# Kernel optimization log

Measured on AMD Instinct MI355X. Metric: run time of the kernel, lower is better.

The kernel has to match this reference:

```python
import jax, jax.numpy as jnp
import numpy as np

N = 4096; E = 32768; S = 64; V = 16; H0 = 64; H1 = 16; STEPS = 3
SQRT3 = float(np.sqrt(3.0))


def _tp(sx, vx, sy, vy):
    # full CG tensor product restricted to paths landing in 0e/1o
    # sx [n,m0], vx [n,m1,3], sy [n,k0], vy [n,k1,3]
    n = sx.shape[0]
    ss = (sx[:, :, None] * sy[:, None, :]).reshape(n, -1)              # 0e x 0e -> 0e
    dd = (jnp.einsum('nmi,nki->nmk', vx, vy) / SQRT3).reshape(n, -1)    # 1o . 1o -> 0e
    sv = (sx[:, :, None, None] * vy[:, None, :, :]).reshape(n, -1, 3)   # 0e x 1o -> 1o
    vs = (vx[:, :, None, :] * sy[:, None, :, None]).reshape(n, -1, 3)   # 1o x 0e -> 1o
    return jnp.concatenate([ss, dd], -1), jnp.concatenate([sv, vs], -2)


def _tpl_gate(sx, vx, sy, vy, ws, b, wv, n0):
    # TensorProductLinearGate: tensor_product -> Linear -> gate
    s_tp, v_tp = _tp(sx, vx, sy, vy)
    s = s_tp @ ws + b                                  # scalars + gate scalars
    v = jnp.einsum('ntd,tm->nmd', v_tp, wv)
    scal = jax.nn.gelu(s[:, :n0])
    gates = jax.nn.sigmoid(s[:, n0:])
    return scal, v * gates[:, :, None]


def _seg_mean(x, idx, n):
    s = jax.ops.segment_sum(x, idx, num_segments=n)
    c = jax.ops.segment_sum(jnp.ones((x.shape[0],), x.dtype), idx, num_segments=n)
    c = jnp.maximum(c, 1.0).reshape((n,) + (1,) * (x.ndim - 1))
    return s / c


def setup_inputs() -> dict:
    key = jax.random.key(0)
    ks = jax.random.split(key, 20)
    f32 = jnp.float32

    def w(k, shape):
        return jax.random.normal(k, shape, f32) / np.sqrt(shape[-2]).astype(np.float32)

    def bias(k, shape):
        return 0.1 * jax.random.normal(k, shape, f32)

    E1 = 2 * (S + V)          # 160: edge block0 TP width
    E2 = H0 + H1              # 80: edge blocks 1-2 TP width
    K0 = H0 + 1; K1 = H1 + 1  # message concat sh
    N0TP = S * K0 + V * K1    # 4432
    N1TP = S * K1 + V * K0    # 2128
    return {
        'node_s': jax.random.normal(ks[0], (N, S), f32),
        'node_v': jax.random.normal(ks[1], (N, V, 3), f32),
        'senders': jax.random.randint(ks[2], (E,), 0, N, jnp.int32),
        'receivers': jax.random.randint(ks[3], (E,), 0, N, jnp.int32),
        'e1_ws': w(ks[4], (STEPS, E1, H0 + H1)),
        'e1_b': bias(ks[5], (STEPS, H0 + H1)),
        'e1_wv': w(ks[6], (STEPS, E1, H1)),
        'e2_ws': w(ks[7], (STEPS, 2, E2, H0 + H1)),
        'e2_b': bias(ks[8], (STEPS, 2, H0 + H1)),
        'e2_wv': w(ks[9], (STEPS, 2, E2, H1)),
        'n_ws': w(ks[10], (STEPS, 3, N0TP, S + V)),
        'n_b': bias(ks[11], (STEPS, 3, S + V)),
        'n_wv': w(ks[12], (STEPS, 3, N1TP, V)),
        'l_ws': w(ks[13], (STEPS, S, S)),
        'l_b': bias(ks[14], (STEPS, S)),
        'l_wv': w(ks[15], (STEPS, V, V)),
    }


def reference(node_s, node_v, senders, receivers, e1_ws, e1_b, e1_wv,
              e2_ws, e2_b, e2_wv, n_ws, n_b, n_wv, l_ws, l_b, l_wv):
    norm = float(E - 1)
    for step in range(STEPS):
        s_i, v_i = node_s[senders], node_v[senders]
        s_j, v_j = node_s[receivers], node_v[receivers]
        r = v_i[:, 0] - v_j[:, 0]                    # slice_by_mul[:1] = positions
        rn = jnp.linalg.norm(r, axis=-1, keepdims=True)
        unit = r / jnp.maximum(rn, 1e-9)
        a_s = jnp.ones((E, 1), node_s.dtype)          # Y_0, component norm
        a_v = (SQRT3 * unit)[:, None, :]              # Y_1, component norm
        m_s = jnp.concatenate([s_i, s_j], -1)
        m_v = jnp.concatenate([v_i, v_j], -2)
        for blk in range(3):
            if blk == 0:
                ws, b, wv = e1_ws[step], e1_b[step], e1_wv[step]
            else:
                ws, b, wv = e2_ws[step, blk - 1], e2_b[step, blk - 1], e2_wv[step, blk - 1]
            m_s, m_v = _tpl_gate(m_s, m_v, a_s, a_v, ws, b, wv, H0)
        # ---- aggregate (segment_mean) + normalize_messages ----
        ms = _seg_mean(m_s, receivers, N) / norm
        mv = _seg_mean(m_v, receivers, N) / norm
        as_ = _seg_mean(a_s, receivers, N) / norm
        av = _seg_mean(a_v, receivers, N) / norm
        y_s = jnp.concatenate([ms, as_], -1)          # [N, H0+1]
        y_v = jnp.concatenate([mv, av], -2)           # [N, H1+1, 3]
        for blk in range(3):
            node_s, node_v = _tpl_gate(node_s, node_v, y_s, y_v,
                                       n_ws[step, blk], n_b[step, blk], n_wv[step, blk], S)
        # ---- final per-step Linear(irreps_in) ----
        node_s = node_s @ l_ws[step] + l_b[step]
        node_v = jnp.einsum('nmd,mk->nkd', node_v, l_wv[step])
    return jnp.concatenate([node_v.reshape(node_v.shape[0], -1), node_s], -1)
```

## Files before the change

kernel.cpp:

```cpp
#include <hip/hip_runtime.h>
#include <math.h>

constexpr int NND = 4096;
constexpr int EDG = 32768;
constexpr float SQRT3  = 1.7320508075688772f;
constexpr float ISQRT3 = 0.5773502691896258f;
constexpr float NORMI  = 1.0f / 32767.0f;

__device__ __forceinline__ float gelu_f(float x) {
    float x3 = x * x * x;
    return 0.5f * x * (1.0f + tanhf(0.7978845608028654f * (x + 0.044715f * x3)));
}
__device__ __forceinline__ float sigmoid_f(float x) {
    return 1.0f / (1.0f + expf(-x));
}

__global__ __launch_bounds__(256)
void segnn_deg_kernel(const int* __restrict__ rcv, int* __restrict__ deg) {
    const int e = blockIdx.x * 256 + threadIdx.x;
    if (e < EDG) atomicAdd(deg + rcv[e], 1);
}

__global__ __launch_bounds__(1024)
void segnn_scan_kernel(const int* __restrict__ deg, int* __restrict__ off) {
    __shared__ int tots[1024];
    const int t = threadIdx.x;
    const int v0 = deg[4*t], v1 = deg[4*t+1], v2 = deg[4*t+2], v3 = deg[4*t+3];
    const int p1 = v0, p2 = p1 + v1, p3 = p2 + v2, p4 = p3 + v3;
    tots[t] = p4;
    __syncthreads();
    for (int d = 1; d < 1024; d <<= 1) {
        const int add = (t >= d) ? tots[t - d] : 0;
        __syncthreads();
        tots[t] += add;
        __syncthreads();
    }
    const int excl = t ? tots[t-1] : 0;
    off[4*t+0] = excl;
    off[4*t+1] = excl + p1;
    off[4*t+2] = excl + p2;
    off[4*t+3] = excl + p3;
    if (t == 1023) off[4096] = tots[1023];
}

__global__ __launch_bounds__(256)
void segnn_scatter_kernel(const int* __restrict__ rcv, const int* __restrict__ off,
                          int* __restrict__ cursor, int* __restrict__ elist) {
    const int e = blockIdx.x * 256 + threadIdx.x;
    if (e < EDG) {
        const int j = rcv[e];
        const int p = atomicAdd(cursor + j, 1);
        elist[off[j] + p] = e;
    }
}

template<int NSX, int NVX>
__device__ __forceinline__ void edge_phase_w(
    const int lane,
    const float* __restrict__ Ws, const float* __restrict__ Bs,
    const float* __restrict__ Wv,
    float (*xt)[10], float (*x2)[10], float (*cb)[96], float (*cvv)[48])
{
    const int cs = lane & 15, kg = lane >> 4;
    constexpr int KA = NSX + NVX;
    constexpr int CH = KA / 4;

    {
        float acc[8][6];
#pragma unroll
        for (int j = 0; j < 8; ++j)
#pragma unroll
            for (int c = 0; c < 6; ++c) acc[j][c] = 0.0f;
        const int r0 = kg * CH;
#pragma unroll 4
        for (int rr = 0; rr < CH; ++rr) {
            const int r = r0 + rr;
            const float* wp = Ws + r*80 + cs;
            const float w0 = wp[0], w1 = wp[16], w2 = wp[32], w3 = wp[48], w4 = wp[64];
            const float w5 = (r < NSX) ? Wv[r*16 + cs] : 0.0f;
            const float2 xa = *reinterpret_cast<const float2*>(&xt[r][0]);
            const float2 xb = *reinterpret_cast<const float2*>(&xt[r][2]);
            const float2 xc = *reinterpret_cast<const float2*>(&xt[r][4]);
            const float2 xd = *reinterpret_cast<const float2*>(&xt[r][6]);
            const float xe[8] = { xa.x,xa.y, xb.x,xb.y, xc.x,xc.y, xd.x,xd.y };
#pragma unroll
            for (int j = 0; j < 8; ++j) {
                acc[j][0] = fmaf(xe[j], w0, acc[j][0]);
                acc[j][1] = fmaf(xe[j], w1, acc[j][1]);
                acc[j][2] = fmaf(xe[j], w2, acc[j][2]);
                acc[j][3] = fmaf(xe[j], w3, acc[j][3]);
                acc[j][4] = fmaf(xe[j], w4, acc[j][4]);
                acc[j][5] = fmaf(xe[j], w5, acc[j][5]);
            }
        }
#pragma unroll
        for (int j = 0; j < 8; ++j)
#pragma unroll
            for (int c = 0; c < 6; ++c) {
                float a = acc[j][c];
                a += __shfl_xor(a, 16);
                a += __shfl_xor(a, 32);
                acc[j][c] = a;
            }
        if (lane < 16) {
#pragma unroll
            for (int j = 0; j < 8; ++j) {
#pragma unroll
                for (int c = 0; c < 5; ++c) cb[j][cs + 16*c] = acc[j][c] + Bs[cs + 16*c];
                cb[j][80 + cs] = acc[j][5];
            }
        }
    }

    {
        constexpr int CHB = NVX / 4;
        float av[8][3];
#pragma unroll
        for (int j = 0; j < 8; ++j) { av[j][0]=0.0f; av[j][1]=0.0f; av[j][2]=0.0f; }
        const int m0 = kg * CHB;
#pragma unroll
        for (int mm = 0; mm < CHB; ++mm) {
            const int m = m0 + mm;
            const float w = Wv[(NSX + m)*16 + cs];
#pragma unroll
            for (int d = 0; d < 3; ++d) {
                const float2 xa = *reinterpret_cast<const float2*>(&x2[d*NVX + m][0]);
                const float2 xb = *reinterpret_cast<const float2*>(&x2[d*NVX + m][2]);
                const float2 xc = *reinterpret_cast<const float2*>(&x2[d*NVX + m][4]);
                const float2 xd = *reinterpret_cast<const float2*>(&x2[d*NVX + m][6]);
                const float xe[8] = { xa.x,xa.y, xb.x,xb.y, xc.x,xc.y, xd.x,xd.y };
#pragma unroll
                for (int j = 0; j < 8; ++j) av[j][d] = fmaf(xe[j], w, av[j][d]);
            }
        }
#pragma unroll
        for (int j = 0; j < 8; ++j)
#pragma unroll
            for (int d = 0; d < 3; ++d) {
                float a = av[j][d];
                a += __shfl_xor(a, 16);
                a += __shfl_xor(a, 32);
                av[j][d] = a;
            }
        if (lane < 16) {
#pragma unroll
            for (int j = 0; j < 8; ++j)
#pragma unroll
                for (int d = 0; d < 3; ++d) cvv[j][cs*3 + d] = av[j][d];
        }
    }
    asm volatile("" ::: "memory");
}

__global__ __launch_bounds__(256, 2)
void segnn_edge_fused(const float* __restrict__ cs, const float* __restrict__ cv,
                      const int* __restrict__ snd, const int* __restrict__ rcv,
                      const float* __restrict__ W0s, const float* __restrict__ B0, const float* __restrict__ W0v,
                      const float* __restrict__ W1s, const float* __restrict__ B1, const float* __restrict__ W1v,
                      const float* __restrict__ W2s, const float* __restrict__ B2, const float* __restrict__ W2v,
                      float* __restrict__ msg) {
    __shared__ __align__(16) float XT [4][160][10];
    __shared__ __align__(16) float X2T[4][96][10];
    __shared__ __align__(16) float Cb [4][8][96];
    __shared__ __align__(16) float Cv [4][8][48];
    __shared__ float UU [4][8][4];

    const int tid  = threadIdx.x;
    const int w    = tid >> 6;
    const int lane = tid & 63;
    const int e0   = blockIdx.x * 32 + w * 8;

    float (*xt)[10]  = XT[w];
    float (*x2)[10]  = X2T[w];
    float (*cb)[96]  = Cb[w];
    float (*cvv)[48] = Cv[w];
    float (*uuw)[4]  = UU[w];

#pragma unroll
    for (int it = 0; it < 16; ++it) {
        const int e = it >> 1, half = it & 1;
        const int node = (half ? rcv : snd)[e0 + e];
        xt[half*64 + lane][e] = cs[(size_t)node*64 + lane];
    }
#pragma unroll
    for (int it = 0; it < 16; ++it) {
        const int e = it >> 1, half = it & 1;
        if (lane < 48) {
            const int node = (half ? rcv : snd)[e0 + e];
            const int m = lane / 3, d = lane - 3*m;
            x2[d*32 + half*16 + m][e] = cv[(size_t)node*48 + lane];
        }
    }
    asm volatile("" ::: "memory");
    if (lane < 8) {
        const float rx = x2[0][lane]  - x2[16][lane];
        const float ry = x2[32][lane] - x2[48][lane];
        const float rz = x2[64][lane] - x2[80][lane];
        const float rinv = 1.0f / fmaxf(sqrtf(rx*rx+ry*ry+rz*rz), 1e-9f);
        uuw[lane][0] = rx*rinv; uuw[lane][1] = ry*rinv; uuw[lane][2] = rz*rinv;
    }
    asm volatile("" ::: "memory");
#pragma unroll
    for (int it = 0; it < 4; ++it) {
        const int idx = it*64 + lane;
        const int e = idx >> 5, mm = idx & 31;
        xt[128 + mm][e] = x2[mm][e]*uuw[e][0] + x2[32+mm][e]*uuw[e][1] + x2[64+mm][e]*uuw[e][2];
    }
    asm volatile("" ::: "memory");

    edge_phase_w<128,32>(lane, W0s, B0, W0v, xt, x2, cb, cvv);
#pragma unroll
    for (int it = 0; it < 8; ++it) {
        xt[lane][it] = gelu_f(cb[it][lane]);
    }
#pragma unroll
    for (int it = 0; it < 2; ++it) {
        const int idx = it*64 + lane;
        const int e = idx >> 4, o = idx & 15;
        const float g = sigmoid_f(cb[e][64+o]);
        const float t = cb[e][80+o] * SQRT3;
        float p = 0.0f;
#pragma unroll
        for (int d = 0; d < 3; ++d) {
            const float vd = fmaf(t, uuw[e][d], cvv[e][o*3+d]) * g;
            x2[d*16 + o][e] = vd;
            p = fmaf(vd, uuw[e][d], p);
        }
        xt[64 + o][e] = p;
    }
    asm volatile("" ::: "memory");

    edge_phase_w<64,16>(lane, W1s, B1, W1v, xt, x2, cb, cvv);
#pragma unroll
    for (int it = 0; it < 8; ++it) {
        xt[lane][it] = gelu_f(cb[it][lane]);
    }
#pragma unroll
    for (int it = 0; it < 2; ++it) {
        const int idx = it*64 + lane;
        const int e = idx >> 4, o = idx & 15;
        const float g = sigmoid_f(cb[e][64+o]);
        const float t = cb[e][80+o] * SQRT3;
        float p = 0.0f;
#pragma unroll
        for (int d = 0; d < 3; ++d) {
            const float vd = fmaf(t, uuw[e][d], cvv[e][o*3+d]) * g;
            x2[d*16 + o][e] = vd;
            p = fmaf(vd, uuw[e][d], p);
        }
        xt[64 + o][e] = p;
    }
    asm volatile("" ::: "memory");

    edge_phase_w<64,16>(lane, W2s, B2, W2v, xt, x2, cb, cvv);
#pragma unroll
    for (int it = 0; it < 15; ++it) {
        const int idx = it*64 + lane;
        if (idx < 920) {
            const int e = idx / 115, f = idx - 115*e;
            float vv;
            if (f < 64) {
                vv = gelu_f(cb[e][f]);
            } else if (f < 112) {
                const int q = f - 64, o = q / 3, d = q - 3*o;
                const float g = sigmoid_f(cb[e][64+o]);
                vv = fmaf(cb[e][80+o] * SQRT3, uuw[e][d], cvv[e][q]) * g;
            } else {
                vv = uuw[e][f-112];
            }
            msg[(size_t)(e0+e)*116 + f] = vv;
        }
    }
}

__global__ __launch_bounds__(128)
void segnn_gather_kernel(const float* __restrict__ msg, const int* __restrict__ off,
                         const int* __restrict__ elist,
                         float* __restrict__ y_s, float* __restrict__ y_v) {
    const int n = blockIdx.x, f = threadIdx.x;
    const int o0 = off[n], o1 = off[n+1];
    const int deg = o1 - o0;
    float acc = 0.0f;
    for (int p = o0; p < o1; ++p) {
        const int eid = elist[p];
        if (f < 115) acc += msg[(size_t)eid*116 + f];
    }
    const float inv = NORMI / (float)(deg > 0 ? deg : 1);
    if (f < 64)        y_s[(size_t)n*65 + f] = acc * inv;
    else if (f < 112)  y_v[(size_t)n*51 + (f-64)] = acc * inv;
    else if (f < 115)  y_v[(size_t)n*51 + 48 + (f-112)] = SQRT3 * acc * inv;
    else if (f == 115) y_s[(size_t)n*65 + 64] = deg ? NORMI : 0.0f;
}

__global__ __launch_bounds__(512, 4)
void segnn_node_kernel(const float* __restrict__ in_s, const float* __restrict__ in_v,
                       const float* __restrict__ y_s, const float* __restrict__ y_v,
                       const float* __restrict__ W,  const float* __restrict__ B,
                       const float* __restrict__ Wv,
                       float* __restrict__ out_s, float* __restrict__ out_v) {
    __shared__ __align__(16) float xsL[8*65];
    __shared__ __align__(16) float ysL[8*65];
    __shared__ __align__(16) float xvL[8*49];
    __shared__ __align__(16) float yvL[8*51];
    __shared__ __align__(16) float Xa[2][3072];
    __shared__ __align__(16) float red[8][16][41];
    __shared__ float finGG[8*16];

    const int tid  = threadIdx.x;
    const int lane = tid & 63;
    const int wv   = tid >> 6;
    const int nb0  = blockIdx.x * 8;

    for (int idx = tid; idx < 8*64; idx += 512) { const int n = idx >> 6, m = idx & 63; xsL[n*65+m] = in_s[(size_t)(nb0+n)*64 + m]; }
    for (int idx = tid; idx < 8*65; idx += 512) { const int n = idx / 65, k = idx - n*65; ysL[n*65+k] = y_s[(size_t)(nb0+n)*65 + k]; }
    for (int idx = tid; idx < 8*48; idx += 512) { const int n = idx / 48, m = idx - n*48; xvL[n*49+m] = in_v[(size_t)(nb0+n)*48 + m]; }
    for (int idx = tid; idx < 8*51; idx += 512) { const int n = idx / 51, m = idx - n*51; yvL[n*51+m] = y_v[(size_t)(nb0+n)*51 + m]; }
    __syncthreads();

    {
        const int cs = tid & 15;
        const int rowgrp = tid >> 4;

        float acc[8][5];
#pragma unroll
        for (int n = 0; n < 8; ++n)
#pragma unroll
            for (int c = 0; c < 5; ++c) acc[n][c] = 0.0f;

        auto genS = [&](int t, int b) {
            const int base = t * 128;
#pragma unroll
            for (int ii = 0; ii < 2; ++ii) {
                const int idx = tid + ii*512;
                const int rl = idx >> 3, n = idx & 7;
                const int r = base + rl;
                float val = 0.0f;
                if (r < 4160) {
                    const int m = r / 65, k = r - m*65;
                    val = xsL[n*65+m] * ysL[n*65+k];
                } else if (r < 4432) {
                    const int q = r - 4160;
                    const int m = q / 17, k = q - m*17;
                    val = (xvL[n*49+m*3+0]*yvL[n*51+k*3+0] +
                           xvL[n*49+m*3+1]*yvL[n*51+k*3+1] +
                           xvL[n*49+m*3+2]*yvL[n*51+k*3+2]) * ISQRT3;
                }
                Xa[b][idx ^ (((idx >> 8) & 3) << 3)] = val;
            }
        };

        genS(0, 0);
        __syncthreads();
        for (int t = 0; t < 35; ++t) {
            if (t + 1 < 35) genS(t + 1, (t + 1) & 1);
            const int base = t * 128;
            const float* Xb = &Xa[t & 1][0];
#pragma unroll
            for (int v2 = 0; v2 < 4; ++v2) {
                const int rl = rowgrp + 32*v2;
                const int r  = base + rl;
                const int wr = r < 4431 ? r : 4431;
                const float* wp = W + (size_t)wr * 80 + cs;
                const float w0 = wp[0], w1 = wp[16], w2 = wp[32], w3 = wp[48], w4_ = wp[64];
                const int sb = (rl*8) ^ (((rl >> 5) & 3) << 3);
                const float4 xq0 = *reinterpret_cast<const float4*>(&Xb[sb]);
                const float4 xq1 = *reinterpret_cast<const float4*>(&Xb[sb+4]);
                const float xn[8] = { xq0.x, xq0.y, xq0.z, xq0.w, xq1.x, xq1.y, xq1.z, xq1.w };
#pragma unroll
                for (int n = 0; n < 8; ++n) {
                    acc[n][0] = fmaf(xn[n], w0,  acc[n][0]);
                    acc[n][1] = fmaf(xn[n], w1,  acc[n][1]);
                    acc[n][2] = fmaf(xn[n], w2,  acc[n][2]);
                    acc[n][3] = fmaf(xn[n], w3,  acc[n][3]);
                    acc[n][4] = fmaf(xn[n], w4_, acc[n][4]);
                }
            }
            __syncthreads();
        }

#pragma unroll
        for (int n = 0; n < 8; ++n)
#pragma unroll
            for (int c = 0; c < 5; ++c) {
                float a = acc[n][c];
                a += __shfl_xor(a, 16);
                a += __shfl_xor(a, 32);
                if (lane < 16) red[wv][lane][n*5+c] = a;
            }
        __syncthreads();
        for (int idx = tid; idx < 8*80; idx += 512) {
            const int n = idx / 80, col = idx - n*80;
            const int cs2 = col & 15, ci2 = col >> 4;
            float s = B[col];
#pragma unroll
            for (int ww = 0; ww < 8; ++ww) s += red[ww][cs2][n*5+ci2];
            if (col < 64) out_s[(size_t)(nb0+n)*64 + col] = gelu_f(s);
            else          finGG[n*16 + (col-64)] = s;
        }
        __syncthreads();
    }

    {
        const int j4 = tid & 3;
        const int ngrp = (tid >> 2) & 1;
        const int rg = tid >> 3;

        float av[12][4];
#pragma unroll
        for (int a = 0; a < 12; ++a)
#pragma unroll
            for (int c = 0; c < 4; ++c) av[a][c] = 0.0f;

        auto genV = [&](int t, int b) {
            const int base = t * 128;
#pragma unroll
            for (int ii = 0; ii < 6; ++ii) {
                const int idx = tid + ii*512;
                const int rl = idx / 24, ar = idx - rl*24;
                const int n = ar / 3, d = ar - n*3;
                const int r = base + rl;
                float val = 0.0f;
                if (r < 1088) {
                    const int m = r / 17, k = r - m*17;
                    val = xsL[n*65+m] * yvL[n*51+k*3+d];
                } else if (r < 2128) {
                    const int q = r - 1088;
                    const int m = q / 65, k = q - m*65;
                    val = xvL[n*49+m*3+d] * ysL[n*65+k];
                }
                Xa[b][idx] = val;
            }
        };

        genV(0, 0);
        __syncthreads();
        for (int t = 0; t < 17; ++t) {
            if (t + 1 < 17) genV(t + 1, (t + 1) & 1);
            const float* Xb = &Xa[t & 1][0];
#pragma unroll
            for (int v2 = 0; v2 < 2; ++v2) {
                const int rl = rg + 64*v2;
                const int r  = t*128 + rl;
                const int wr = r < 2127 ? r : 2127;
                const float4 w4 = *reinterpret_cast<const float4*>(&Wv[(size_t)wr*16 + 4*j4]);
                const float4 xq0 = *reinterpret_cast<const float4*>(&Xb[rl*24 + 12*ngrp]);
                const float4 xq1 = *reinterpret_cast<const float4*>(&Xb[rl*24 + 12*ngrp + 4]);
                const float4 xq2 = *reinterpret_cast<const float4*>(&Xb[rl*24 + 12*ngrp + 8]);
                const float xr[12] = { xq0.x,xq0.y,xq0.z,xq0.w, xq1.x,xq1.y,xq1.z,xq1.w, xq2.x,xq2.y,xq2.z,xq2.w };
#pragma unroll
                for (int a = 0; a < 12; ++a) {
                    av[a][0] = fmaf(xr[a], w4.x, av[a][0]);
                    av[a][1] = fmaf(xr[a], w4.y, av[a][1]);
                    av[a][2] = fmaf(xr[a], w4.z, av[a][2]);
                    av[a][3] = fmaf(xr[a], w4.w, av[a][3]);
                }
            }
            __syncthreads();
        }

        float* redf = &red[0][0][0];
#pragma unroll
        for (int a = 0; a < 12; ++a)
#pragma unroll
            for (int c = 0; c < 4; ++c) {
                float x = av[a][c];
                x += __shfl_xor(x, 8);
                x += __shfl_xor(x, 16);
                x += __shfl_xor(x, 32);
                if (lane < 8) redf[wv*392 + lane*49 + a*4 + c] = x;
            }
        __syncthreads();
        for (int idx = tid; idx < 24*16; idx += 512) {
            const int ar = idx >> 4, j = idx & 15;
            const int n = ar / 3, d = ar - n*3;
            const int ng2 = ar / 12, a2 = ar - 12*ng2;
            const int jj4 = j >> 2, c2 = j & 3;
            float s = 0.0f;
#pragma unroll
            for (int ww = 0; ww < 8; ++ww) s += redf[ww*392 + (jj4 + 4*ng2)*49 + a2*4 + c2];
            out_v[(size_t)(nb0+n)*48 + j*3 + d] = s * sigmoid_f(finGG[n*16 + j]);
        }
    }
}

__global__ __launch_bounds__(256)
void segnn_linear_kernel(const float* __restrict__ in_s, const float* __restrict__ in_v,
                         const float* __restrict__ lws, const float* __restrict__ lb,
                         const float* __restrict__ lwv,
                         float* __restrict__ out_s, float* __restrict__ out_v,
                         float* __restrict__ out_cat) {
    const int idx = blockIdx.x * 256 + threadIdx.x;
    if (idx >= NND * 112) return;
    const int nidx = idx / 112, f = idx - nidx * 112;
    if (f < 48) {
        const int k = f / 3, d = f - 3*k;
        const float* vp = in_v + (size_t)nidx * 48 + d;
        float acc = 0.0f;
#pragma unroll
        for (int m = 0; m < 16; ++m) acc = fmaf(vp[m*3], lwv[m*16 + k], acc);
        if (out_cat) out_cat[(size_t)nidx*112 + f] = acc;
        else         out_v[(size_t)nidx*48 + f] = acc;
    } else {
        const int o = f - 48;
        const float* sp = in_s + (size_t)nidx * 64;
        float acc = lb[o];
#pragma unroll
        for (int m = 0; m < 64; ++m) acc = fmaf(sp[m], lws[m*64 + o], acc);
        if (out_cat) out_cat[(size_t)nidx*112 + f] = acc;
        else         out_s[(size_t)nidx*64 + o] = acc;
    }
}

extern "C" void kernel_launch(void* const* d_in, const int* in_sizes, int n_in,
                              void* d_out, int out_size, void* d_ws, size_t ws_size,
                              hipStream_t stream) {
    const float* in_s  = (const float*)d_in[0];
    const float* in_v  = (const float*)d_in[1];
    const int*   snd   = (const int*)  d_in[2];
    const int*   rcv   = (const int*)  d_in[3];
    const float* e1_ws = (const float*)d_in[4];
    const float* e1_b  = (const float*)d_in[5];
    const float* e1_wv = (const float*)d_in[6];
    const float* e2_ws = (const float*)d_in[7];
    const float* e2_b  = (const float*)d_in[8];
    const float* e2_wv = (const float*)d_in[9];
    const float* n_ws  = (const float*)d_in[10];
    const float* n_b   = (const float*)d_in[11];
    const float* n_wv  = (const float*)d_in[12];
    const float* l_ws  = (const float*)d_in[13];
    const float* l_b   = (const float*)d_in[14];
    const float* l_wv  = (const float*)d_in[15];

    float* ws    = (float*)d_ws;
    float* cur_s = ws;
    float* cur_v = cur_s + 262144;
    float* nxt_s = cur_v + 196608;
    float* nxt_v = nxt_s + 262144;
    float* y_s   = nxt_v + 196608;
    float* y_v   = y_s + 266240;
    float* msg   = y_v + 208896;
    int*   deg    = (int*)(msg + 3801088);
    int*   cursor = deg + 4096;
    int*   off    = cursor + 4096;
    int*   elist  = off + 4097;

    hipMemsetAsync(deg, 0, (size_t)8192 * sizeof(int), stream);
    hipMemcpyAsync(cur_s, in_s, (size_t)262144 * sizeof(float), hipMemcpyDeviceToDevice, stream);
    hipMemcpyAsync(cur_v, in_v, (size_t)196608 * sizeof(float), hipMemcpyDeviceToDevice, stream);
    segnn_deg_kernel<<<EDG/256, 256, 0, stream>>>(rcv, deg);
    segnn_scan_kernel<<<1, 1024, 0, stream>>>(deg, off);
    segnn_scatter_kernel<<<EDG/256, 256, 0, stream>>>(rcv, off, cursor, elist);

    for (int step = 0; step < 3; ++step) {
        segnn_edge_fused<<<EDG/32, 256, 0, stream>>>(cur_s, cur_v, snd, rcv,
            e1_ws + (size_t)step*160*80, e1_b + step*80, e1_wv + (size_t)step*160*16,
            e2_ws + (size_t)(step*2+0)*80*80, e2_b + (step*2+0)*80, e2_wv + (size_t)(step*2+0)*80*16,
            e2_ws + (size_t)(step*2+1)*80*80, e2_b + (step*2+1)*80, e2_wv + (size_t)(step*2+1)*80*16,
            msg);
        segnn_gather_kernel<<<NND, 128, 0, stream>>>(msg, off, elist, y_s, y_v);

        segnn_node_kernel<<<NND/8, 512, 0, stream>>>(cur_s, cur_v, y_s, y_v,
            n_ws + (size_t)(step*3+0)*4432*80, n_b + (step*3+0)*80, n_wv + (size_t)(step*3+0)*2128*16,
            nxt_s, nxt_v);
        segnn_node_kernel<<<NND/8, 512, 0, stream>>>(nxt_s, nxt_v, y_s, y_v,
            n_ws + (size_t)(step*3+1)*4432*80, n_b + (step*3+1)*80, n_wv + (size_t)(step*3+1)*2128*16,
            cur_s, cur_v);
        segnn_node_kernel<<<NND/8, 512, 0, stream>>>(cur_s, cur_v, y_s, y_v,
            n_ws + (size_t)(step*3+2)*4432*80, n_b + (step*3+2)*80, n_wv + (size_t)(step*3+2)*2128*16,
            nxt_s, nxt_v);

        segnn_linear_kernel<<<(NND*112 + 255)/256, 256, 0, stream>>>(nxt_s, nxt_v,
            l_ws + (size_t)step*64*64, l_b + step*64, l_wv + (size_t)step*16*16,
            cur_s, cur_v, (step == 2) ? (float*)d_out : nullptr);
    }
}
```

Measured before the change: 1.065 ms.

## Process 16 nodes per block in node kernel to halve weight reloads

The node TP-linear-gate kernel now handles 16 nodes per block instead of 8, so each weight row loaded from global memory is reused across twice as many nodes. Accumulator count per thread doubles (80 floats for the scalar path), the vector path is re-tiled to 64 rows per stage, and the cross-wave reduction now runs in two phases to fit in shared memory. Shared-memory row paddings change and the XOR swizzle is dropped. The trade-off is higher register pressure with launch bounds (512,4), which may cause spills or lower occupancy, and only half as many blocks are launched.

```diff
diff --git a/kernel.cpp b/kernel.cpp
--- a/kernel.cpp
+++ b/kernel.cpp
@@ -298,54 +298,54 @@
                        const float* __restrict__ W,  const float* __restrict__ B,
                        const float* __restrict__ Wv,
                        float* __restrict__ out_s, float* __restrict__ out_v) {
-    __shared__ __align__(16) float xsL[8*65];
-    __shared__ __align__(16) float ysL[8*65];
-    __shared__ __align__(16) float xvL[8*49];
-    __shared__ __align__(16) float yvL[8*51];
+    __shared__ __align__(16) float xsL[16*66];
+    __shared__ __align__(16) float ysL[16*68];
+    __shared__ __align__(16) float xvL[16*49];
+    __shared__ __align__(16) float yvL[16*52];
     __shared__ __align__(16) float Xa[2][3072];
-    __shared__ __align__(16) float red[8][16][41];
-    __shared__ float finGG[8*16];
+    __shared__ __align__(16) float red[4][16][81];
+    __shared__ float finGG[16*16];
 
     const int tid  = threadIdx.x;
     const int lane = tid & 63;
     const int wv   = tid >> 6;
-    const int nb0  = blockIdx.x * 8;
-
-    for (int idx = tid; idx < 8*64; idx += 512) { const int n = idx >> 6, m = idx & 63; xsL[n*65+m] = in_s[(size_t)(nb0+n)*64 + m]; }
-    for (int idx = tid; idx < 8*65; idx += 512) { const int n = idx / 65, k = idx - n*65; ysL[n*65+k] = y_s[(size_t)(nb0+n)*65 + k]; }
-    for (int idx = tid; idx < 8*48; idx += 512) { const int n = idx / 48, m = idx - n*48; xvL[n*49+m] = in_v[(size_t)(nb0+n)*48 + m]; }
-    for (int idx = tid; idx < 8*51; idx += 512) { const int n = idx / 51, m = idx - n*51; yvL[n*51+m] = y_v[(size_t)(nb0+n)*51 + m]; }
+    const int nb0  = blockIdx.x * 16;
+
+    for (int idx = tid; idx < 16*64; idx += 512) { const int n = idx >> 6, m = idx & 63; xsL[n*66+m] = in_s[(size_t)(nb0+n)*64 + m]; }
+    for (int idx = tid; idx < 16*65; idx += 512) { const int n = idx / 65, k = idx - n*65; ysL[n*68+k] = y_s[(size_t)(nb0+n)*65 + k]; }
+    for (int idx = tid; idx < 16*48; idx += 512) { const int n = idx / 48, m = idx - n*48; xvL[n*49+m] = in_v[(size_t)(nb0+n)*48 + m]; }
+    for (int idx = tid; idx < 16*51; idx += 512) { const int n = idx / 51, m = idx - n*51; yvL[n*52+m] = y_v[(size_t)(nb0+n)*51 + m]; }
     __syncthreads();
 
     {
         const int cs = tid & 15;
         const int rowgrp = tid >> 4;
 
-        float acc[8][5];
-#pragma unroll
-        for (int n = 0; n < 8; ++n)
+        float acc[16][5];
+#pragma unroll
+        for (int n = 0; n < 16; ++n)
 #pragma unroll
             for (int c = 0; c < 5; ++c) acc[n][c] = 0.0f;
 
         auto genS = [&](int t, int b) {
             const int base = t * 128;
 #pragma unroll
-            for (int ii = 0; ii < 2; ++ii) {
+            for (int ii = 0; ii < 4; ++ii) {
                 const int idx = tid + ii*512;
-                const int rl = idx >> 3, n = idx & 7;
+                const int rl = idx >> 4, n = idx & 15;
                 const int r = base + rl;
                 float val = 0.0f;
                 if (r < 4160) {
                     const int m = r / 65, k = r - m*65;
-                    val = xsL[n*65+m] * ysL[n*65+k];
+                    val = xsL[n*66+m] * ysL[n*68+k];
                 } else if (r < 4432) {
                     const int q = r - 4160;
                     const int m = q / 17, k = q - m*17;
-                    val = (xvL[n*49+m*3+0]*yvL[n*51+k*3+0] +
-                           xvL[n*49+m*3+1]*yvL[n*51+k*3+1] +
-                           xvL[n*49+m*3+2]*yvL[n*51+k*3+2]) * ISQRT3;
+                    val = (xvL[n*49+m*3+0]*yvL[n*52+k*3+0] +
+                           xvL[n*49+m*3+1]*yvL[n*52+k*3+1] +
+                           xvL[n*49+m*3+2]*yvL[n*52+k*3+2]) * ISQRT3;
                 }
-                Xa[b][idx ^ (((idx >> 8) & 3) << 3)] = val;
+                Xa[b][idx] = val;
             }
         };
 
@@ -362,12 +362,14 @@
                 const int wr = r < 4431 ? r : 4431;
                 const float* wp = W + (size_t)wr * 80 + cs;
                 const float w0 = wp[0], w1 = wp[16], w2 = wp[32], w3 = wp[48], w4_ = wp[64];
-                const int sb = (rl*8) ^ (((rl >> 5) & 3) << 3);
-                const float4 xq0 = *reinterpret_cast<const float4*>(&Xb[sb]);
-                const float4 xq1 = *reinterpret_cast<const float4*>(&Xb[sb+4]);
-                const float xn[8] = { xq0.x, xq0.y, xq0.z, xq0.w, xq1.x, xq1.y, xq1.z, xq1.w };
-#pragma unroll
-                for (int n = 0; n < 8; ++n) {
+                const float4 xq0 = *reinterpret_cast<const float4*>(&Xb[rl*16]);
+                const float4 xq1 = *reinterpret_cast<const float4*>(&Xb[rl*16+4]);
+                const float4 xq2 = *reinterpret_cast<const float4*>(&Xb[rl*16+8]);
+                const float4 xq3 = *reinterpret_cast<const float4*>(&Xb[rl*16+12]);
+                const float xn[16] = { xq0.x,xq0.y,xq0.z,xq0.w, xq1.x,xq1.y,xq1.z,xq1.w,
+                                       xq2.x,xq2.y,xq2.z,xq2.w, xq3.x,xq3.y,xq3.z,xq3.w };
+#pragma unroll
+                for (int n = 0; n < 16; ++n) {
                     acc[n][0] = fmaf(xn[n], w0,  acc[n][0]);
                     acc[n][1] = fmaf(xn[n], w1,  acc[n][1]);
                     acc[n][2] = fmaf(xn[n], w2,  acc[n][2]);
@@ -379,21 +381,34 @@
         }
 
 #pragma unroll
-        for (int n = 0; n < 8; ++n)
+        for (int n = 0; n < 16; ++n)
 #pragma unroll
             for (int c = 0; c < 5; ++c) {
                 float a = acc[n][c];
                 a += __shfl_xor(a, 16);
                 a += __shfl_xor(a, 32);
-                if (lane < 16) red[wv][lane][n*5+c] = a;
-            }
-        __syncthreads();
-        for (int idx = tid; idx < 8*80; idx += 512) {
+                acc[n][c] = a;
+            }
+        if (lane < 16 && wv < 4) {
+#pragma unroll
+            for (int n = 0; n < 16; ++n)
+#pragma unroll
+                for (int c = 0; c < 5; ++c) red[wv][lane][n*5+c] = acc[n][c];
+        }
+        __syncthreads();
+        if (lane < 16 && wv >= 4) {
+#pragma unroll
+            for (int n = 0; n < 16; ++n)
+#pragma unroll
+                for (int c = 0; c < 5; ++c) red[wv-4][lane][n*5+c] += acc[n][c];
+        }
+        __syncthreads();
+        for (int idx = tid; idx < 16*80; idx += 512) {
             const int n = idx / 80, col = idx - n*80;
             const int cs2 = col & 15, ci2 = col >> 4;
             float s = B[col];
 #pragma unroll
-            for (int ww = 0; ww < 8; ++ww) s += red[ww][cs2][n*5+ci2];
+            for (int ww = 0; ww < 4; ++ww) s += red[ww][cs2][n*5+ci2];
             if (col < 64) out_s[(size_t)(nb0+n)*64 + col] = gelu_f(s);
             else          finGG[n*16 + (col-64)] = s;
         }
@@ -401,9 +416,9 @@
     }
 
     {
-        const int j4 = tid & 3;
-        const int ngrp = (tid >> 2) & 1;
-        const int rg = tid >> 3;
+        const int j4   = tid & 3;
+        const int agrp = (tid >> 2) & 3;
+        const int rg   = tid >> 4;
 
         float av[12][4];
 #pragma unroll
@@ -412,21 +427,21 @@
             for (int c = 0; c < 4; ++c) av[a][c] = 0.0f;
 
         auto genV = [&](int t, int b) {
-            const int base = t * 128;
+            const int base = t * 64;
 #pragma unroll
             for (int ii = 0; ii < 6; ++ii) {
                 const int idx = tid + ii*512;
-                const int rl = idx / 24, ar = idx - rl*24;
+                const int rl = idx / 48, ar = idx - rl*48;
                 const int n = ar / 3, d = ar - n*3;
                 const int r = base + rl;
                 float val = 0.0f;
                 if (r < 1088) {
                     const int m = r / 17, k = r - m*17;
-                    val = xsL[n*65+m] * yvL[n*51+k*3+d];
+                    val = xsL[n*66+m] * yvL[n*52+k*3+d];
                 } else if (r < 2128) {
                     const int q = r - 1088;
                     const int m = q / 65, k = q - m*65;
-                    val = xvL[n*49+m*3+d] * ysL[n*65+k];
+                    val = xvL[n*49+m*3+d] * ysL[n*68+k];
                 }
                 Xa[b][idx] = val;
             }
@@ -434,18 +449,18 @@
 
         genV(0, 0);
         __syncthreads();
-        for (int t = 0; t < 17; ++t) {
-            if (t + 1 < 17) genV(t + 1, (t + 1) & 1);
+        for (int t = 0; t < 34; ++t) {
+            if (t + 1 < 34) genV(t + 1, (t + 1) & 1);
             const float* Xb = &Xa[t & 1][0];
 #pragma unroll
             for (int v2 = 0; v2 < 2; ++v2) {
-                const int rl = rg + 64*v2;
-                const int r  = t*128 + rl;
+                const int rl = rg + 32*v2;
+                const int r  = t*64 + rl;
                 const int wr = r < 2127 ? r : 2127;
                 const float4 w4 = *reinterpret_cast<const float4*>(&Wv[(size_t)wr*16 + 4*j4]);
-                const float4 xq0 = *reinterpret_cast<const float4*>(&Xb[rl*24 + 12*ngrp]);
-                const float4 xq1 = *reinterpret_cast<const float4*>(&Xb[rl*24 + 12*ngrp + 4]);
-                const float4 xq2 = *reinterpret_cast<const float4*>(&Xb[rl*24 + 12*ngrp + 8]);
+                const float4 xq0 = *reinterpret_cast<const float4*>(&Xb[rl*48 + 12*agrp]);
+                const float4 xq1 = *reinterpret_cast<const float4*>(&Xb[rl*48 + 12*agrp + 4]);
+                const float4 xq2 = *reinterpret_cast<const float4*>(&Xb[rl*48 + 12*agrp + 8]);
                 const float xr[12] = { xq0.x,xq0.y,xq0.z,xq0.w, xq1.x,xq1.y,xq1.z,xq1.w, xq2.x,xq2.y,xq2.z,xq2.w };
 #pragma unroll
                 for (int a = 0; a < 12; ++a) {
@@ -464,21 +479,34 @@
 #pragma unroll
             for (int c = 0; c < 4; ++c) {
                 float x = av[a][c];
-                x += __shfl_xor(x, 8);
                 x += __shfl_xor(x, 16);
                 x += __shfl_xor(x, 32);
-                if (lane < 8) redf[wv*392 + lane*49 + a*4 + c] = x;
-            }
-        __syncthreads();
-        for (int idx = tid; idx < 24*16; idx += 512) {
-            const int ar = idx >> 4, j = idx & 15;
+                av[a][c] = x;
+            }
+        if (lane < 16 && wv < 4) {
+#pragma unroll
+            for (int a = 0; a < 12; ++a)
+#pragma unroll
+                for (int c = 0; c < 4; ++c) redf[wv*784 + lane*49 + a*4 + c] = av[a][c];
+        }
+        __syncthreads();
+        if (lane < 16 && wv >= 4) {
+#pragma unroll
+            for (int a = 0; a < 12; ++a)
+#pragma unroll
+                for (int c = 0; c < 4; ++c) redf[(wv-4)*784 + lane*49 + a*4 + c] += av[a][c];
+        }
+        __syncthreads();
+        for (int idx = tid; idx < 48*16; idx += 512) {
+            const int ar = idx >> 4, col = idx & 15;
             const int n = ar / 3, d = ar - n*3;
-            const int ng2 = ar / 12, a2 = ar - 12*ng2;
-            const int jj4 = j >> 2, c2 = j & 3;
+            const int ag2 = ar / 12, a2 = ar - 12*ag2;
+            const int jj4 = col >> 2, c2 = col & 3;
+            const int lane2 = ag2*4 + jj4;
             float s = 0.0f;
 #pragma unroll
-            for (int ww = 0; ww < 8; ++ww) s += redf[ww*392 + (jj4 + 4*ng2)*49 + a2*4 + c2];
-            out_v[(size_t)(nb0+n)*48 + j*3 + d] = s * sigmoid_f(finGG[n*16 + j]);
+            for (int ww = 0; ww < 4; ++ww) s += redf[ww*784 + lane2*49 + a2*4 + c2];
+            out_v[(size_t)(nb0+n)*48 + col*3 + d] = s * sigmoid_f(finGG[n*16 + col]);
         }
     }
 }
@@ -559,13 +587,13 @@
             msg);
         segnn_gather_kernel<<<NND, 128, 0, stream>>>(msg, off, elist, y_s, y_v);
 
-        segnn_node_kernel<<<NND/8, 512, 0, stream>>>(cur_s, cur_v, y_s, y_v,
+        segnn_node_kernel<<<NND/16, 512, 0, stream>>>(cur_s, cur_v, y_s, y_v,
             n_ws + (size_t)(step*3+0)*4432*80, n_b + (step*3+0)*80, n_wv + (size_t)(step*3+0)*2128*16,
             nxt_s, nxt_v);
-        segnn_node_kernel<<<NND/8, 512, 0, stream>>>(nxt_s, nxt_v, y_s, y_v,
+        segnn_node_kernel<<<NND/16, 512, 0, stream>>>(nxt_s, nxt_v, y_s, y_v,
             n_ws + (size_t)(step*3+1)*4432*80, n_b + (step*3+1)*80, n_wv + (size_t)(step*3+1)*2128*16,
             cur_s, cur_v);
-        segnn_node_kernel<<<NND/8, 512, 0, stream>>>(cur_s, cur_v, y_s, y_v,
+        segnn_node_kernel<<<NND/16, 512, 0, stream>>>(cur_s, cur_v, y_s, y_v,
             n_ws + (size_t)(step*3+2)*4432*80, n_b + (step*3+2)*80, n_wv + (size_t)(step*3+2)*2128*16,
             nxt_s, nxt_v);
 
```

Result: slower. 2.764 ms (+159.5%).

## Raise node kernel occupancy target, halve reduction buffer, drop Xa swizzle

Applied to the files above, without the earlier changes.

The node kernel's launch bounds now ask for 6 blocks per CU instead of 4, which tightens the register budget per thread. The cross-wave reduction buffer is halved: waves 4-7 add their partials into the slots written by waves 0-3, with one extra barrier, to cut LDS use per block. The XOR swizzle on the Xa staging buffer is removed, and the ysL/yvL rows are padded to 68 and 52 floats. The aim is more resident waves per CU. The risk is register spilling on the large accumulator arrays and new LDS bank conflicts where the swizzle used to prevent them.

```diff
diff --git a/kernel.cpp b/kernel.cpp
--- a/kernel.cpp
+++ b/kernel.cpp
@@ -292,18 +292,18 @@
     else if (f == 115) y_s[(size_t)n*65 + 64] = deg ? NORMI : 0.0f;
 }
 
-__global__ __launch_bounds__(512, 4)
+__global__ __launch_bounds__(512, 6)
 void segnn_node_kernel(const float* __restrict__ in_s, const float* __restrict__ in_v,
                        const float* __restrict__ y_s, const float* __restrict__ y_v,
                        const float* __restrict__ W,  const float* __restrict__ B,
                        const float* __restrict__ Wv,
                        float* __restrict__ out_s, float* __restrict__ out_v) {
     __shared__ __align__(16) float xsL[8*65];
-    __shared__ __align__(16) float ysL[8*65];
+    __shared__ __align__(16) float ysL[8*68];
     __shared__ __align__(16) float xvL[8*49];
-    __shared__ __align__(16) float yvL[8*51];
+    __shared__ __align__(16) float yvL[8*52];
     __shared__ __align__(16) float Xa[2][3072];
-    __shared__ __align__(16) float red[8][16][41];
+    __shared__ __align__(16) float red[4][16][41];
     __shared__ float finGG[8*16];
 
     const int tid  = threadIdx.x;
@@ -312,9 +312,9 @@
     const int nb0  = blockIdx.x * 8;
 
     for (int idx = tid; idx < 8*64; idx += 512) { const int n = idx >> 6, m = idx & 63; xsL[n*65+m] = in_s[(size_t)(nb0+n)*64 + m]; }
-    for (int idx = tid; idx < 8*65; idx += 512) { const int n = idx / 65, k = idx - n*65; ysL[n*65+k] = y_s[(size_t)(nb0+n)*65 + k]; }
+    for (int idx = tid; idx < 8*65; idx += 512) { const int n = idx / 65, k = idx - n*65; ysL[n*68+k] = y_s[(size_t)(nb0+n)*65 + k]; }
     for (int idx = tid; idx < 8*48; idx += 512) { const int n = idx / 48, m = idx - n*48; xvL[n*49+m] = in_v[(size_t)(nb0+n)*48 + m]; }
-    for (int idx = tid; idx < 8*51; idx += 512) { const int n = idx / 51, m = idx - n*51; yvL[n*51+m] = y_v[(size_t)(nb0+n)*51 + m]; }
+    for (int idx = tid; idx < 8*51; idx += 512) { const int n = idx / 51, m = idx - n*51; yvL[n*52+m] = y_v[(size_t)(nb0+n)*51 + m]; }
     __syncthreads();
 
     {
@@ -337,15 +337,15 @@
                 float val = 0.0f;
                 if (r < 4160) {
                     const int m = r / 65, k = r - m*65;
-                    val = xsL[n*65+m] * ysL[n*65+k];
+                    val = xsL[n*65+m] * ysL[n*68+k];
                 } else if (r < 4432) {
                     const int q = r - 4160;
                     const int m = q / 17, k = q - m*17;
-                    val = (xvL[n*49+m*3+0]*yvL[n*51+k*3+0] +
-                           xvL[n*49+m*3+1]*yvL[n*51+k*3+1] +
-                           xvL[n*49+m*3+2]*yvL[n*51+k*3+2]) * ISQRT3;
+                    val = (xvL[n*49+m*3+0]*yvL[n*52+k*3+0] +
+                           xvL[n*49+m*3+1]*yvL[n*52+k*3+1] +
+                           xvL[n*49+m*3+2]*yvL[n*52+k*3+2]) * ISQRT3;
                 }
-                Xa[b][idx ^ (((idx >> 8) & 3) << 3)] = val;
+                Xa[b][idx] = val;
             }
         };
 
@@ -362,9 +362,8 @@
                 const int wr = r < 4431 ? r : 4431;
                 const float* wp = W + (size_t)wr * 80 + cs;
                 const float w0 = wp[0], w1 = wp[16], w2 = wp[32], w3 = wp[48], w4_ = wp[64];
-                const int sb = (rl*8) ^ (((rl >> 5) & 3) << 3);
-                const float4 xq0 = *reinterpret_cast<const float4*>(&Xb[sb]);
-                const float4 xq1 = *reinterpret_cast<const float4*>(&Xb[sb+4]);
+                const float4 xq0 = *reinterpret_cast<const float4*>(&Xb[rl*8]);
+                const float4 xq1 = *reinterpret_cast<const float4*>(&Xb[rl*8+4]);
                 const float xn[8] = { xq0.x, xq0.y, xq0.z, xq0.w, xq1.x, xq1.y, xq1.z, xq1.w };
 #pragma unroll
                 for (int n = 0; n < 8; ++n) {
@@ -385,15 +384,28 @@
                 float a = acc[n][c];
                 a += __shfl_xor(a, 16);
                 a += __shfl_xor(a, 32);
-                if (lane < 16) red[wv][lane][n*5+c] = a;
-            }
+                acc[n][c] = a;
+            }
+        if (lane < 16 && wv < 4) {
+#pragma unroll
+            for (int n = 0; n < 8; ++n)
+#pragma unroll
+                for (int c = 0; c < 5; ++c) red[wv][lane][n*5+c] = acc[n][c];
+        }
+        __syncthreads();
+        if (lane < 16 && wv >= 4) {
+#pragma unroll
+            for (int n = 0; n < 8; ++n)
+#pragma unroll
+                for (int c = 0; c < 5; ++c) red[wv-4][lane][n*5+c] += acc[n][c];
+        }
         __syncthreads();
         for (int idx = tid; idx < 8*80; idx += 512) {
             const int n = idx / 80, col = idx - n*80;
             const int cs2 = col & 15, ci2 = col >> 4;
             float s = B[col];
 #pragma unroll
-            for (int ww = 0; ww < 8; ++ww) s += red[ww][cs2][n*5+ci2];
+            for (int ww = 0; ww < 4; ++ww) s += red[ww][cs2][n*5+ci2];
             if (col < 64) out_s[(size_t)(nb0+n)*64 + col] = gelu_f(s);
             else          finGG[n*16 + (col-64)] = s;
         }
@@ -422,11 +434,11 @@
                 float val = 0.0f;
                 if (r < 1088) {
                     const int m = r / 17, k = r - m*17;
-                    val = xsL[n*65+m] * yvL[n*51+k*3+d];
+                    val = xsL[n*65+m] * yvL[n*52+k*3+d];
                 } else if (r < 2128) {
                     const int q = r - 1088;
                     const int m = q / 65, k = q - m*65;
-                    val = xvL[n*49+m*3+d] * ysL[n*65+k];
+                    val = xvL[n*49+m*3+d] * ysL[n*68+k];
                 }
                 Xa[b][idx] = val;
             }
@@ -467,8 +479,21 @@
                 x += __shfl_xor(x, 8);
                 x += __shfl_xor(x, 16);
                 x += __shfl_xor(x, 32);
-                if (lane < 8) redf[wv*392 + lane*49 + a*4 + c] = x;
-            }
+                av[a][c] = x;
+            }
+        if (lane < 8 && wv < 4) {
+#pragma unroll
+            for (int a = 0; a < 12; ++a)
+#pragma unroll
+                for (int c = 0; c < 4; ++c) redf[wv*392 + lane*49 + a*4 + c] = av[a][c];
+        }
+        __syncthreads();
+        if (lane < 8 && wv >= 4) {
+#pragma unroll
+            for (int a = 0; a < 12; ++a)
+#pragma unroll
+                for (int c = 0; c < 4; ++c) redf[(wv-4)*392 + lane*49 + a*4 + c] += av[a][c];
+        }
         __syncthreads();
         for (int idx = tid; idx < 24*16; idx += 512) {
             const int ar = idx >> 4, j = idx & 15;
@@ -477,7 +502,7 @@
             const int jj4 = j >> 2, c2 = j & 3;
             float s = 0.0f;
 #pragma unroll
-            for (int ww = 0; ww < 8; ++ww) s += redf[ww*392 + (jj4 + 4*ng2)*49 + a2*4 + c2];
+            for (int ww = 0; ww < 4; ++ww) s += redf[ww*392 + (jj4 + 4*ng2)*49 + a2*4 + c2];
             out_v[(size_t)(nb0+n)*48 + j*3 + d] = s * sigmoid_f(finGG[n*16 + j]);
         }
     }
```

After: 1.700 ms. +59.6%, slower.
